# Performance work log

Hardware: AMD Instinct MI355X
Metric: run time of the kernel (lower is better)

The kernel has to match this reference:

```python
import jax, jax.numpy as jnp
import numpy as np

# static config (matches init_kwargs)
B = 16
S = 32          # patch grid side
td = 2          # tile_dim
ts = td * td    # tile size
T = (S // td) ** 2
R = 1           # register tokens
U = 1           # tile_comp_size
P = S * S
N = R + P
KC = T * U
K = R + KC
D = 768
H = 12
DH = D // H
HID = 32        # CPB hidden


def setup_inputs() -> dict:
    key = jax.random.key(0)
    ks = jax.random.split(key, 11)
    sc = 0.02
    x = jax.random.normal(ks[0], (B, N, D), jnp.float32)
    logit_w = jax.random.normal(ks[1], (U, D), jnp.float32) * sc
    q_w = jax.random.normal(ks[2], (D, D), jnp.float32) * sc
    kv_w = jax.random.normal(ks[3], (2 * D, D), jnp.float32) * sc
    out_w = jax.random.normal(ks[4], (D, D), jnp.float32) * sc
    out_b = jax.random.normal(ks[5], (D,), jnp.float32) * sc
    cpb_w1 = jax.random.normal(ks[6], (HID, 3), jnp.float32) * 0.5
    cpb_b1 = jax.random.normal(ks[7], (HID,), jnp.float32) * sc
    cpb_w2 = jax.random.normal(ks[8], (H, HID), jnp.float32) * 0.1
    cpb_b2 = jax.random.normal(ks[9], (H,), jnp.float32) * sc
    u_pos = jax.random.normal(ks[10], (1, U, 3), jnp.float32) * sc
    # query patch positions [qx, qy, 0] on the SxS grid (row-major)
    coords = np.arange(S, dtype=np.float32)
    gy, gx = np.meshgrid(coords, coords, indexing='ij')
    P_pos = np.stack([gx.ravel(), gy.ravel(), np.zeros(P, np.float32)], axis=-1)[:, None, :]
    # per-tile centers [cx, cy, 0], tile index t = row_tile*(S//td)+col_tile
    tc = np.arange(S // td, dtype=np.float32) * td + (td - 1) / 2.0
    ty, tx = np.meshgrid(tc, tc, indexing='ij')
    tile_centers = np.stack([tx.ravel(), ty.ravel(), np.zeros(T, np.float32)], axis=-1)[:, None, :]
    return {
        'x': x, 'logit_w': logit_w, 'q_w': q_w, 'kv_w': kv_w,
        'out_w': out_w, 'out_b': out_b,
        'cpb_w1': cpb_w1, 'cpb_b1': cpb_b1, 'cpb_w2': cpb_w2, 'cpb_b2': cpb_b2,
        'u_pos': u_pos,
        'P_pos': jnp.asarray(P_pos), 'tile_centers': jnp.asarray(tile_centers),
    }


def _cpb_bias(P_pos, tile_centers, u_pos, cpb_w1, cpb_b1, cpb_w2, cpb_b2, dtype):
    # anchors: tile center + tied per-U offset -> [KC, 3]
    k_pos = (tile_centers + u_pos).reshape(KC, 3)
    delta = P_pos - k_pos[None, :, :].reshape(1, KC, 3)  # [P, KC, 3]
    dxy, s_feat = delta[..., :2], delta[..., 2:]
    phi_xy = jnp.sign(dxy) * jnp.log1p(jnp.abs(dxy))
    feats = jnp.concatenate([phi_xy, -s_feat], axis=-1)  # [P, KC, 3]
    h = jax.nn.gelu(feats @ cpb_w1.T + cpb_b1, approximate=False)
    out_ctx = h @ cpb_w2.T + cpb_b2  # [P, KC, H]
    bias = jnp.zeros((N, K, H), dtype).at[R:, R:, :].set(out_ctx.astype(dtype))
    return bias.transpose(2, 0, 1)  # [H, N, K]


def reference(x, logit_w, q_w, kv_w, out_w, out_b,
              cpb_w1, cpb_b1, cpb_w2, cpb_b2, u_pos, P_pos, tile_centers):
    Bx = x.shape[0]
    # --- tiled softmax-weighted compression ---
    patch = x[:, R:, :].reshape(Bx, S // td, td, S // td, td, D)
    tiled = patch.transpose(0, 1, 3, 2, 4, 5).reshape(Bx, T, ts, D)  # [B,T,ts,D]
    scores = jnp.einsum('btsd,ud->btsu', tiled, logit_w)             # [B,T,ts,U]
    w = jax.nn.softmax(scores.astype(jnp.float32).transpose(0, 1, 3, 2), axis=-1)
    w = w.astype(scores.dtype)                                       # [B,T,U,ts]
    ctx_learn = jnp.einsum('btus,btsd->btud', w, tiled).reshape(Bx, T * U, D)
    ctx = jnp.concatenate([x[:, :R, :], ctx_learn], axis=1)          # [B,K,D]
    # --- projections ---
    q = jnp.einsum('bnd,ed->bne', x, q_w).reshape(Bx, N, H, DH).transpose(0, 2, 1, 3)
    kv = jnp.einsum('bkd,ed->bke', ctx, kv_w).reshape(Bx, K, 2, H, DH)
    k = kv[:, :, 0].transpose(0, 2, 1, 3)  # [B,H,K,DH]
    v = kv[:, :, 1].transpose(0, 2, 1, 3)
    # --- CPB additive bias + SDPA ---
    bias = _cpb_bias(P_pos, tile_centers, u_pos, cpb_w1, cpb_b1, cpb_w2, cpb_b2, x.dtype)
    scale = DH ** -0.5
    logits = jnp.einsum('bhnd,bhkd->bhnk', q, k) * scale + bias[None]
    attn = jax.nn.softmax(logits, axis=-1)
    o = jnp.einsum('bhnk,bhkd->bhnd', attn, v).transpose(0, 2, 1, 3).reshape(Bx, N, D)
    return o @ out_w.T + out_b
```

## Files before the change

kernel.cpp:

```cpp
#include <hip/hip_runtime.h>
#include <math.h>

namespace {
constexpr int BB   = 16;
constexpr int SS   = 32;
constexpr int TT   = 256;
constexpr int PP   = 1024;
constexpr int NTOK = 1025;
constexpr int KCC  = 256;
constexpr int KTOK = 257;
constexpr int DD   = 768;
constexpr int HH   = 12;
constexpr int DHH  = 64;
constexpr int BNP  = 1040;
}

typedef _Float16 f16x8 __attribute__((ext_vector_type(8)));
typedef _Float16 f16x2 __attribute__((ext_vector_type(2)));
typedef float f32x4 __attribute__((ext_vector_type(4)));

#define GLOAD_LDS16(gsrc, ldst)                                               \
  __builtin_amdgcn_global_load_lds(                                           \
      (const __attribute__((address_space(1))) unsigned int*)(gsrc),          \
      (__attribute__((address_space(3))) unsigned int*)(ldst), 16, 0, 0)

__global__ __launch_bounds__(256) void cvt_weights_kernel(
    const float* __restrict__ q_w, const float* __restrict__ kv_w,
    const float* __restrict__ out_w,
    _Float16* __restrict__ qwh, _Float16* __restrict__ kvwh,
    _Float16* __restrict__ owh) {
  constexpr int NQ = DD * DD;
  constexpr int NK = 2 * DD * DD;
  const int i = (blockIdx.x * 256 + threadIdx.x) * 8;
  const float* src;
  _Float16* dst;
  int off;
  float scale = 1.0f;
  if (i < NQ) { src = q_w; dst = qwh; off = i; scale = 0.125f; }
  else if (i < NQ + NK) { src = kv_w; dst = kvwh; off = i - NQ; }
  else if (i < NQ + NK + NQ) { src = out_w; dst = owh; off = i - NQ - NK; }
  else return;
  const float4 a = *(const float4*)(src + off);
  const float4 b = *(const float4*)(src + off + 4);
  f16x8 o;
  o[0] = (_Float16)(a.x * scale); o[1] = (_Float16)(a.y * scale);
  o[2] = (_Float16)(a.z * scale); o[3] = (_Float16)(a.w * scale);
  o[4] = (_Float16)(b.x * scale); o[5] = (_Float16)(b.y * scale);
  o[6] = (_Float16)(b.z * scale); o[7] = (_Float16)(b.w * scale);
  *(f16x8*)(dst + off) = o;
}

__global__ __launch_bounds__(256) void ctx_kernel(
    const float* __restrict__ x, const float* __restrict__ logit_w,
    _Float16* __restrict__ ctxh, _Float16* __restrict__ xh) {
  const int blk = blockIdx.x;
  const int b = blk >> 8;
  const int t = blk & 255;
  const int tid = threadIdx.x;
  const int lane = tid & 63;
  const int w = tid >> 6;
  const float* xb = x + (size_t)b * NTOK * DD;
  _Float16* xhb = xh + (size_t)b * NTOK * DD;

  int prow[4];
#pragma unroll
  for (int s = 0; s < 4; ++s)
    prow[s] = 1 + ((t >> 4) * 2 + (s >> 1)) * SS + ((t & 15) * 2 + (s & 1));

  float sv[3][4];
  float part[4] = {0.f, 0.f, 0.f, 0.f};
#pragma unroll
  for (int it = 0; it < 3; ++it) {
    const int d = tid + 256 * it;
    const float lw = logit_w[d];
#pragma unroll
    for (int s = 0; s < 4; ++s) {
      const float xv = xb[(size_t)prow[s] * DD + d];
      sv[it][s] = xv;
      part[s] += xv * lw;
      xhb[(size_t)prow[s] * DD + d] = (_Float16)xv;
    }
  }

#pragma unroll
  for (int dd = 1; dd < 64; dd <<= 1)
#pragma unroll
    for (int s = 0; s < 4; ++s) part[s] += __shfl_xor(part[s], dd, 64);
  __shared__ float wred[4][4];
  if (lane == 0)
#pragma unroll
    for (int s = 0; s < 4; ++s) wred[w][s] = part[s];
  __syncthreads();
  float score[4];
#pragma unroll
  for (int s = 0; s < 4; ++s)
    score[s] = wred[0][s] + wred[1][s] + wred[2][s] + wred[3][s];

  const float mx = fmaxf(fmaxf(score[0], score[1]), fmaxf(score[2], score[3]));
  float e[4], sum = 0.f;
#pragma unroll
  for (int s = 0; s < 4; ++s) { e[s] = expf(score[s] - mx); sum += e[s]; }
  const float inv = 1.f / sum;
#pragma unroll
  for (int s = 0; s < 4; ++s) e[s] *= inv;

  _Float16* crow = ctxh + ((size_t)b * KTOK + 1 + t) * DD;
#pragma unroll
  for (int it = 0; it < 3; ++it) {
    const int d = tid + 256 * it;
    float acc = 0.f;
#pragma unroll
    for (int s = 0; s < 4; ++s) acc += e[s] * sv[it][s];
    crow[d] = (_Float16)acc;
  }
  if (t == 0) {
    _Float16* dst = ctxh + (size_t)b * KTOK * DD;
#pragma unroll
    for (int it = 0; it < 3; ++it) {
      const int d = tid + 256 * it;
      const float xv = xb[d];
      dst[d] = (_Float16)xv;
      xhb[d] = (_Float16)xv;
    }
  }
}

template <int OUTF16>
__global__ __launch_bounds__(256) void gemm_f16_kernel(
    const _Float16* __restrict__ A, const _Float16* __restrict__ W,
    const float* __restrict__ bias, void* __restrict__ Cout,
    int M, int Nout, int gx) {
  constexpr int BK = 64;
  __shared__ _Float16 As[128 * BK];
  __shared__ _Float16 Ws[128 * BK];

  const int tid = threadIdx.x;
  const int lane = tid & 63;
  const int w = tid >> 6;
  const int fr = lane & 15;
  const int g = lane >> 4;
  const int awm = (w >> 1) * 64;
  const int awn = (w & 1) * 64;

  const int nwg = gridDim.x;
  const int q8 = nwg >> 3, r8 = nwg & 7;
  const int xcd = blockIdx.x & 7;
  const int base = (xcd < r8) ? xcd * (q8 + 1) : r8 * (q8 + 1) + (xcd - r8) * q8;
  const int wg = base + (blockIdx.x >> 3);
  const int row0 = (wg / gx) * 128;
  const int col0 = (wg % gx) * 128;

  const int srow = lane >> 3;
  const int schunk = (lane & 7) ^ (srow & 7);

  f32x4 acc[4][4];
#pragma unroll
  for (int i = 0; i < 4; ++i)
#pragma unroll
    for (int j = 0; j < 4; ++j) acc[i][j] = (f32x4){0.f, 0.f, 0.f, 0.f};

  for (int k0 = 0; k0 < 768; k0 += BK) {
    __syncthreads();
#pragma unroll
    for (int c = 0; c < 4; ++c) {
      const int rl = w * 32 + c * 8 + srow;
      int ga = row0 + rl;
      ga = ga < M ? ga : M - 1;
      GLOAD_LDS16(A + (size_t)ga * 768 + k0 + schunk * 8, &As[(w * 32 + c * 8) * BK]);
      GLOAD_LDS16(W + (size_t)(col0 + rl) * 768 + k0 + schunk * 8,
                  &Ws[(w * 32 + c * 8) * BK]);
    }
    __syncthreads();

#pragma unroll
    for (int ks = 0; ks < 2; ++ks) {
      f16x8 af[4], bf[4];
#pragma unroll
      for (int i = 0; i < 4; ++i) {
        const int row = awm + i * 16 + fr;
        af[i] = *(const f16x8*)&As[row * BK + (((ks * 4 + g) ^ (fr & 7)) * 8)];
      }
#pragma unroll
      for (int j = 0; j < 4; ++j) {
        const int row = awn + j * 16 + fr;
        bf[j] = *(const f16x8*)&Ws[row * BK + (((ks * 4 + g) ^ (fr & 7)) * 8)];
      }
#pragma unroll
      for (int i = 0; i < 4; ++i)
#pragma unroll
        for (int j = 0; j < 4; ++j)
          acc[i][j] = __builtin_amdgcn_mfma_f32_16x16x32_f16(af[i], bf[j], acc[i][j], 0, 0, 0);
    }
  }

#pragma unroll
  for (int i = 0; i < 4; ++i) {
    const int rbase = row0 + awm + i * 16 + g * 4;
#pragma unroll
    for (int reg = 0; reg < 4; ++reg) {
      const int gr = rbase + reg;
      if (gr >= M) continue;
      if constexpr (OUTF16) {
        _Float16* crow = (_Float16*)Cout + (size_t)gr * Nout + col0;
#pragma unroll
        for (int j = 0; j < 4; ++j)
          crow[awn + j * 16 + fr] = (_Float16)acc[i][j][reg];
      } else {
        float* crow = (float*)Cout + (size_t)gr * Nout + col0;
#pragma unroll
        for (int j = 0; j < 4; ++j) {
          const int gc = awn + j * 16 + fr;
          crow[gc] = acc[i][j][reg] + bias[col0 + gc];
        }
      }
    }
  }
}

__global__ __launch_bounds__(256) void cpb_kernel(
    const float* __restrict__ P_pos, const float* __restrict__ tile_centers,
    const float* __restrict__ u_pos,
    const float* __restrict__ w1, const float* __restrict__ b1,
    const float* __restrict__ w2, const float* __restrict__ b2,
    float* __restrict__ biasK) {
  const int idx = blockIdx.x * 256 + threadIdx.x;
  const int c = idx >> 10;
  const int p = idx & 1023;

  const float px = P_pos[p * 3 + 0], py = P_pos[p * 3 + 1], pz = P_pos[p * 3 + 2];
  const float kx = tile_centers[c * 3 + 0] + u_pos[0];
  const float ky = tile_centers[c * 3 + 1] + u_pos[1];
  const float kz = tile_centers[c * 3 + 2] + u_pos[2];
  const float dx = px - kx, dy = py - ky, dz = pz - kz;
  const float fx = copysignf(log1pf(fabsf(dx)), dx);
  const float fy = copysignf(log1pf(fabsf(dy)), dy);
  const float fz = -dz;

  float outh[HH];
#pragma unroll
  for (int h = 0; h < HH; ++h) outh[h] = b2[h];
  for (int j = 0; j < 32; ++j) {
    float hj = fx * w1[j * 3 + 0] + fy * w1[j * 3 + 1] + fz * w1[j * 3 + 2] + b1[j];
    hj = 0.5f * hj * (1.f + erff(hj * 0.70710678118654752f));
#pragma unroll
    for (int h = 0; h < HH; ++h) outh[h] += hj * w2[h * 32 + j];
  }
#pragma unroll
  for (int h = 0; h < HH; ++h) {
    float* row = biasK + ((size_t)h * KCC + c) * BNP;
    row[1 + p] = outh[h];
    if (p == 0) row[0] = 0.f;
    if (p < BNP - 1 - PP) row[1 + PP + p] = 0.f;
  }
}

__global__ __launch_bounds__(256) void attn_mfma_kernel(
    const _Float16* __restrict__ qf, const _Float16* __restrict__ kvf,
    const float* __restrict__ biasK, _Float16* __restrict__ of) {
  __shared__ _Float16 Kh[64 * 64];
  __shared__ _Float16 Vt[64 * 64];
  __shared__ _Float16 Pl[4][16 * 64];

  const int tid = threadIdx.x;
  const int lane = tid & 63;
  const int w = tid >> 6;
  const int fr = lane & 15;
  const int g = lane >> 4;

  const int bid = blockIdx.x;
  const int xcd = bid & 7;
  const int slot = bid >> 3;
  const int j9 = slot / 9;
  const int m = slot - 9 * j9;
  const int grp = xcd + 8 * j9;
  const int b = grp / HH;
  const int h = grp % HH;
  const int q0 = m * 128;

  f16x8 qa[2][2];
#pragma unroll
  for (int i = 0; i < 2; ++i) {
    const int qrow = min(q0 + w * 32 + i * 16 + fr, NTOK - 1);
    const _Float16* src = qf + ((size_t)b * NTOK + qrow) * DD + h * DHH;
#pragma unroll
    for (int ks = 0; ks < 2; ++ks)
      qa[i][ks] = *(const f16x8*)(src + ks * 32 + g * 8);
  }

  float mr_[2][4], lr_[2][4];
#pragma unroll
  for (int i = 0; i < 2; ++i)
#pragma unroll
    for (int r = 0; r < 4; ++r) { mr_[i][r] = -3.0e38f; lr_[i][r] = 0.f; }
  f32x4 outacc[2][4];
#pragma unroll
  for (int i = 0; i < 2; ++i)
#pragma unroll
    for (int j = 0; j < 4; ++j) outacc[i][j] = (f32x4){0.f, 0.f, 0.f, 0.f};

  const int ksr = tid >> 2;
  const int kc0 = (tid & 3) * 2;
  const int vkp = tid & 31;
  const int vdh = (tid >> 5) * 8;
  const int s7 = ksr & 7;

  for (int kt = 0; kt < 4; ++kt) {
    const int k0 = kt * 64;
    __syncthreads();
    {
      const int key = k0 + ksr;
      const _Float16* srcK = kvf + ((size_t)b * KTOK + key) * (2 * DD) + h * DHH;
      *(f16x8*)&Kh[ksr * 64 + ((kc0 ^ s7) * 8)] = *(const f16x8*)(srcK + kc0 * 8);
      *(f16x8*)&Kh[ksr * 64 + (((kc0 + 1) ^ s7) * 8)] = *(const f16x8*)(srcK + kc0 * 8 + 8);
      const int kv0 = k0 + 2 * vkp;
      const f16x8 va = *(const f16x8*)(kvf + ((size_t)b * KTOK + kv0) * (2 * DD) + DD + h * DHH + vdh);
      const f16x8 vbv = *(const f16x8*)(kvf + ((size_t)b * KTOK + kv0 + 1) * (2 * DD) + DD + h * DHH + vdh);
#pragma unroll
      for (int e = 0; e < 8; ++e) {
        const int d = vdh + e;
        f16x2 pr; pr[0] = va[e]; pr[1] = vbv[e];
        *(f16x2*)&Vt[d * 64 + (((vkp >> 2) ^ (d & 7)) * 8) + 2 * (vkp & 3)] = pr;
      }
    }
    __syncthreads();

#pragma unroll
    for (int i = 0; i < 2; ++i) {
      f32x4 sf[4];
      __builtin_amdgcn_s_setprio(1);
#pragma unroll
      for (int f = 0; f < 4; ++f) {
        sf[f] = (f32x4){0.f, 0.f, 0.f, 0.f};
#pragma unroll
        for (int ks = 0; ks < 2; ++ks) {
          const f16x8 kf = *(const f16x8*)&Kh[(f * 16 + fr) * 64 + (((ks * 4 + g) ^ (fr & 7)) * 8)];
          sf[f] = __builtin_amdgcn_mfma_f32_16x16x32_f16(qa[i][ks], kf, sf[f], 0, 0, 0);
        }
      }
      __builtin_amdgcn_s_setprio(0);

      const int nb = min(q0 + w * 32 + i * 16 + g * 4, PP);
      float pm[4][4];
#pragma unroll
      for (int f = 0; f < 4; ++f) {
        const int key = k0 + f * 16 + fr;
        const int cl = min(max(key - 1, 0), KCC - 1);
        const f32x4 b4 = *(const f32x4*)&biasK[((size_t)h * KCC + cl) * BNP + nb];
        const float bm = (key >= 1) ? 1.f : 0.f;
#pragma unroll
        for (int r = 0; r < 4; ++r) pm[f][r] = sf[f][r] + bm * b4[r];
      }

#pragma unroll
      for (int r = 0; r < 4; ++r) {
        float rm = fmaxf(fmaxf(pm[0][r], pm[1][r]), fmaxf(pm[2][r], pm[3][r]));
#pragma unroll
        for (int d = 1; d < 16; d <<= 1) rm = fmaxf(rm, __shfl_xor(rm, d, 64));
        const float mn = fmaxf(mr_[i][r], rm);
        const float corr = __expf(mr_[i][r] - mn);
        mr_[i][r] = mn;
        float rs = 0.f;
#pragma unroll
        for (int f = 0; f < 4; ++f) {
          const float pv = __expf(pm[f][r] - mn);
          pm[f][r] = pv;
          rs += pv;
        }
#pragma unroll
        for (int d = 1; d < 16; d <<= 1) rs += __shfl_xor(rs, d, 64);
        lr_[i][r] = lr_[i][r] * corr + rs;
#pragma unroll
        for (int j = 0; j < 4; ++j) outacc[i][j][r] *= corr;
      }

#pragma unroll
      for (int f = 0; f < 4; ++f)
#pragma unroll
        for (int r = 0; r < 4; ++r) {
          const int prw = g * 4 + r;
          Pl[w][prw * 64 + (((2 * f + (fr >> 3)) ^ (prw & 7)) * 8) + (fr & 7)] =
              (_Float16)pm[f][r];
        }

      __builtin_amdgcn_s_setprio(1);
#pragma unroll
      for (int ks = 0; ks < 2; ++ks) {
        const f16x8 pa = *(const f16x8*)&Pl[w][fr * 64 + (((ks * 4 + g) ^ (fr & 7)) * 8)];
#pragma unroll
        for (int j = 0; j < 4; ++j) {
          const f16x8 vbf = *(const f16x8*)&Vt[(j * 16 + fr) * 64 + (((ks * 4 + g) ^ (fr & 7)) * 8)];
          outacc[i][j] = __builtin_amdgcn_mfma_f32_16x16x32_f16(pa, vbf, outacc[i][j], 0, 0, 0);
        }
      }
      __builtin_amdgcn_s_setprio(0);
    }
  }

  __syncthreads();
  {
    if (ksr < 16) {
      const int key = min(256 + ksr, KTOK - 1);
      const _Float16* srcK = kvf + ((size_t)b * KTOK + key) * (2 * DD) + h * DHH;
      *(f16x8*)&Kh[ksr * 64 + ((kc0 ^ s7) * 8)] = *(const f16x8*)(srcK + kc0 * 8);
      *(f16x8*)&Kh[ksr * 64 + (((kc0 + 1) ^ s7) * 8)] = *(const f16x8*)(srcK + kc0 * 8 + 8);
    }
    if (vkp < 16) {
      const int kv0 = min(256 + 2 * vkp, KTOK - 1);
      const int kv1 = min(256 + 2 * vkp + 1, KTOK - 1);
      const f16x8 va = *(const f16x8*)(kvf + ((size_t)b * KTOK + kv0) * (2 * DD) + DD + h * DHH + vdh);
      const f16x8 vbv = *(const f16x8*)(kvf + ((size_t)b * KTOK + kv1) * (2 * DD) + DD + h * DHH + vdh);
#pragma unroll
      for (int e = 0; e < 8; ++e) {
        const int d = vdh + e;
        f16x2 pr; pr[0] = va[e]; pr[1] = vbv[e];
        *(f16x2*)&Vt[d * 64 + (((vkp >> 2) ^ (d & 7)) * 8) + 2 * (vkp & 3)] = pr;
      }
    }
  }
  __syncthreads();

#pragma unroll
  for (int i = 0; i < 2; ++i) {
    f32x4 sf0 = (f32x4){0.f, 0.f, 0.f, 0.f};
#pragma unroll
    for (int ks = 0; ks < 2; ++ks) {
      const f16x8 kf = *(const f16x8*)&Kh[fr * 64 + (((ks * 4 + g) ^ (fr & 7)) * 8)];
      sf0 = __builtin_amdgcn_mfma_f32_16x16x32_f16(qa[i][ks], kf, sf0, 0, 0, 0);
    }
    const int nb = min(q0 + w * 32 + i * 16 + g * 4, PP);
    const f32x4 b4 = *(const f32x4*)&biasK[((size_t)h * KCC + (KCC - 1)) * BNP + nb];
    float pm0[4];
#pragma unroll
    for (int r = 0; r < 4; ++r)
      pm0[r] = (fr == 0) ? (sf0[r] + b4[r]) : -3.0e38f;

#pragma unroll
    for (int r = 0; r < 4; ++r) {
      float rm = pm0[r];
#pragma unroll
      for (int d = 1; d < 16; d <<= 1) rm = fmaxf(rm, __shfl_xor(rm, d, 64));
      const float mn = fmaxf(mr_[i][r], rm);
      const float corr = __expf(mr_[i][r] - mn);
      mr_[i][r] = mn;
      float pv = __expf(pm0[r] - mn);
      pm0[r] = pv;
      float rs = pv;
#pragma unroll
      for (int d = 1; d < 16; d <<= 1) rs += __shfl_xor(rs, d, 64);
      lr_[i][r] = lr_[i][r] * corr + rs;
#pragma unroll
      for (int j = 0; j < 4; ++j) outacc[i][j][r] *= corr;
    }

#pragma unroll
    for (int r = 0; r < 4; ++r) {
      const int prw = g * 4 + r;
      Pl[w][prw * 64 + (((fr >> 3) ^ (prw & 7)) * 8) + (fr & 7)] = (_Float16)pm0[r];
      Pl[w][prw * 64 + (((2 + (fr >> 3)) ^ (prw & 7)) * 8) + (fr & 7)] = (_Float16)0.f;
    }

    const f16x8 pa = *(const f16x8*)&Pl[w][fr * 64 + ((g ^ (fr & 7)) * 8)];
#pragma unroll
    for (int j = 0; j < 4; ++j) {
      const f16x8 vbf = *(const f16x8*)&Vt[(j * 16 + fr) * 64 + ((g ^ (fr & 7)) * 8)];
      outacc[i][j] = __builtin_amdgcn_mfma_f32_16x16x32_f16(pa, vbf, outacc[i][j], 0, 0, 0);
    }
  }

#pragma unroll
  for (int i = 0; i < 2; ++i)
#pragma unroll
    for (int r = 0; r < 4; ++r) {
      const int n = q0 + w * 32 + i * 16 + g * 4 + r;
      if (n >= NTOK) continue;
      const float inv = 1.f / lr_[i][r];
      _Float16* orow = of + ((size_t)b * NTOK + n) * DD + h * DHH + fr;
#pragma unroll
      for (int j = 0; j < 4; ++j) orow[j * 16] = (_Float16)(outacc[i][j][r] * inv);
    }
}

extern "C" void kernel_launch(void* const* d_in, const int* in_sizes, int n_in,
                              void* d_out, int out_size, void* d_ws, size_t ws_size,
                              hipStream_t stream) {
  const float* x            = (const float*)d_in[0];
  const float* logit_w      = (const float*)d_in[1];
  const float* q_w          = (const float*)d_in[2];
  const float* kv_w         = (const float*)d_in[3];
  const float* out_w        = (const float*)d_in[4];
  const float* out_b        = (const float*)d_in[5];
  const float* cpb_w1       = (const float*)d_in[6];
  const float* cpb_b1       = (const float*)d_in[7];
  const float* cpb_w2       = (const float*)d_in[8];
  const float* cpb_b2       = (const float*)d_in[9];
  const float* u_pos        = (const float*)d_in[10];
  const float* P_pos        = (const float*)d_in[11];
  const float* tile_centers = (const float*)d_in[12];
  float* out = (float*)d_out;

  const int Mq  = BB * NTOK;
  const int Mkv = BB * KTOK;

  char* p = (char*)d_ws;
  auto alloc = [&](size_t bytes) {
    char* r = p;
    p += (bytes + 255) & ~(size_t)255;
    return r;
  };
  _Float16* xh    = (_Float16*)alloc((size_t)Mq * DD * 2);
  _Float16* ctxh  = (_Float16*)alloc((size_t)Mkv * DD * 2);
  _Float16* qwh   = (_Float16*)alloc((size_t)DD * DD * 2);
  _Float16* kvwh  = (_Float16*)alloc((size_t)2 * DD * DD * 2);
  _Float16* owh   = (_Float16*)alloc((size_t)DD * DD * 2);
  _Float16* qbuf  = (_Float16*)alloc((size_t)Mq * DD * 2);
  _Float16* kvbuf = (_Float16*)alloc((size_t)Mkv * 2 * DD * 2);
  float*    biasK = (float*)alloc((size_t)HH * KCC * BNP * 4);
  _Float16* obuf  = (_Float16*)alloc((size_t)Mq * DD * 2);

  const int n_wt = 4 * DD * DD;

  cvt_weights_kernel<<<(n_wt / 8 + 255) / 256, 256, 0, stream>>>(
      q_w, kv_w, out_w, qwh, kvwh, owh);

  ctx_kernel<<<BB * TT, 256, 0, stream>>>(x, logit_w, ctxh, xh);

  const int gq = 6 * 129;
  const int gk = 12 * 33;
  gemm_f16_kernel<1><<<gq, 256, 0, stream>>>(xh, qwh, nullptr, qbuf, Mq, DD, 6);
  gemm_f16_kernel<1><<<gk, 256, 0, stream>>>(ctxh, kvwh, nullptr, kvbuf, Mkv, 2 * DD, 12);

  cpb_kernel<<<(PP * KCC) / 256, 256, 0, stream>>>(
      P_pos, tile_centers, u_pos, cpb_w1, cpb_b1, cpb_w2, cpb_b2, biasK);

  attn_mfma_kernel<<<8 * 216, 256, 0, stream>>>(
      qbuf, kvbuf, biasK, obuf);

  gemm_f16_kernel<0><<<gq, 256, 0, stream>>>(obuf, owh, out_b, out, Mq, DD, 6);
}
```

Baseline: 215.2 us.

## Load full per-head K/V once into LDS and loop waves over query chunks

The attention kernel now launches one 512-thread block per (batch, head). It stages all 257 keys and the transposed values in LDS once, with one barrier, and each of the 8 waves then loops over 16-row query chunks. This removes the repeated K/V loads and the per-tile barriers that every 128-query block paid. In exchange the grid shrinks to 192 blocks on a GPU with many CUs, and LDS use grows to about 88KB per block, which lowers occupancy and leaves the last chunk round unevenly balanced.

```diff
diff --git a/kernel.cpp b/kernel.cpp
--- a/kernel.cpp
+++ b/kernel.cpp
@@ -254,12 +254,14 @@
   }
 }
 
-__global__ __launch_bounds__(256) void attn_mfma_kernel(
+__global__ __launch_bounds__(512) void attn_mfma_kernel(
     const _Float16* __restrict__ qf, const _Float16* __restrict__ kvf,
     const float* __restrict__ biasK, _Float16* __restrict__ of) {
-  __shared__ _Float16 Kh[64 * 64];
-  __shared__ _Float16 Vt[64 * 64];
-  __shared__ _Float16 Pl[4][16 * 64];
+  __shared__ _Float16 Kh[4][64 * 64];
+  __shared__ _Float16 Kt[16 * 64];
+  __shared__ _Float16 Vt[4][64 * 64];
+  __shared__ _Float16 Vtt[64 * 64];
+  __shared__ _Float16 Pl[8][16 * 64];
 
   const int tid = threadIdx.x;
   const int lane = tid & 63;
@@ -267,65 +269,79 @@
   const int fr = lane & 15;
   const int g = lane >> 4;
 
-  const int bid = blockIdx.x;
-  const int xcd = bid & 7;
-  const int slot = bid >> 3;
-  const int j9 = slot / 9;
-  const int m = slot - 9 * j9;
-  const int grp = xcd + 8 * j9;
-  const int b = grp / HH;
-  const int h = grp % HH;
-  const int q0 = m * 128;
-
-  f16x8 qa[2][2];
-#pragma unroll
-  for (int i = 0; i < 2; ++i) {
-    const int qrow = min(q0 + w * 32 + i * 16 + fr, NTOK - 1);
-    const _Float16* src = qf + ((size_t)b * NTOK + qrow) * DD + h * DHH;
-#pragma unroll
-    for (int ks = 0; ks < 2; ++ks)
-      qa[i][ks] = *(const f16x8*)(src + ks * 32 + g * 8);
-  }
-
-  float mr_[2][4], lr_[2][4];
-#pragma unroll
-  for (int i = 0; i < 2; ++i)
-#pragma unroll
-    for (int r = 0; r < 4; ++r) { mr_[i][r] = -3.0e38f; lr_[i][r] = 0.f; }
-  f32x4 outacc[2][4];
-#pragma unroll
-  for (int i = 0; i < 2; ++i)
-#pragma unroll
-    for (int j = 0; j < 4; ++j) outacc[i][j] = (f32x4){0.f, 0.f, 0.f, 0.f};
-
-  const int ksr = tid >> 2;
-  const int kc0 = (tid & 3) * 2;
-  const int vkp = tid & 31;
-  const int vdh = (tid >> 5) * 8;
-  const int s7 = ksr & 7;
-
-  for (int kt = 0; kt < 4; ++kt) {
-    const int k0 = kt * 64;
-    __syncthreads();
-    {
-      const int key = k0 + ksr;
+  const int b = blockIdx.x / HH;
+  const int h = blockIdx.x % HH;
+
+  if (tid < 256) {
+    const int ksr = tid >> 2;
+    const int kc0 = (tid & 3) * 2;
+    const int s7 = ksr & 7;
+#pragma unroll
+    for (int kt = 0; kt < 4; ++kt) {
+      const int key = kt * 64 + ksr;
       const _Float16* srcK = kvf + ((size_t)b * KTOK + key) * (2 * DD) + h * DHH;
-      *(f16x8*)&Kh[ksr * 64 + ((kc0 ^ s7) * 8)] = *(const f16x8*)(srcK + kc0 * 8);
-      *(f16x8*)&Kh[ksr * 64 + (((kc0 + 1) ^ s7) * 8)] = *(const f16x8*)(srcK + kc0 * 8 + 8);
-      const int kv0 = k0 + 2 * vkp;
+      *(f16x8*)&Kh[kt][ksr * 64 + ((kc0 ^ s7) * 8)] = *(const f16x8*)(srcK + kc0 * 8);
+      *(f16x8*)&Kh[kt][ksr * 64 + (((kc0 + 1) ^ s7) * 8)] = *(const f16x8*)(srcK + kc0 * 8 + 8);
+    }
+    if (ksr < 16) {
+      const int key = min(256 + ksr, KTOK - 1);
+      const _Float16* srcK = kvf + ((size_t)b * KTOK + key) * (2 * DD) + h * DHH;
+      *(f16x8*)&Kt[ksr * 64 + ((kc0 ^ s7) * 8)] = *(const f16x8*)(srcK + kc0 * 8);
+      *(f16x8*)&Kt[ksr * 64 + (((kc0 + 1) ^ s7) * 8)] = *(const f16x8*)(srcK + kc0 * 8 + 8);
+    }
+  } else {
+    const int t2 = tid - 256;
+    const int vkp = t2 & 31;
+    const int vdh = (t2 >> 5) * 8;
+#pragma unroll
+    for (int kt = 0; kt < 4; ++kt) {
+      const int kv0 = kt * 64 + 2 * vkp;
       const f16x8 va = *(const f16x8*)(kvf + ((size_t)b * KTOK + kv0) * (2 * DD) + DD + h * DHH + vdh);
       const f16x8 vbv = *(const f16x8*)(kvf + ((size_t)b * KTOK + kv0 + 1) * (2 * DD) + DD + h * DHH + vdh);
 #pragma unroll
       for (int e = 0; e < 8; ++e) {
         const int d = vdh + e;
         f16x2 pr; pr[0] = va[e]; pr[1] = vbv[e];
-        *(f16x2*)&Vt[d * 64 + (((vkp >> 2) ^ (d & 7)) * 8) + 2 * (vkp & 3)] = pr;
-      }
-    }
-    __syncthreads();
-
-#pragma unroll
-    for (int i = 0; i < 2; ++i) {
+        *(f16x2*)&Vt[kt][d * 64 + (((vkp >> 2) ^ (d & 7)) * 8) + 2 * (vkp & 3)] = pr;
+      }
+    }
+    if (vkp < 16) {
+      const int kv0 = min(256 + 2 * vkp, KTOK - 1);
+      const int kv1 = min(256 + 2 * vkp + 1, KTOK - 1);
+      const f16x8 va = *(const f16x8*)(kvf + ((size_t)b * KTOK + kv0) * (2 * DD) + DD + h * DHH + vdh);
+      const f16x8 vbv = *(const f16x8*)(kvf + ((size_t)b * KTOK + kv1) * (2 * DD) + DD + h * DHH + vdh);
+#pragma unroll
+      for (int e = 0; e < 8; ++e) {
+        const int d = vdh + e;
+        f16x2 pr; pr[0] = va[e]; pr[1] = vbv[e];
+        *(f16x2*)&Vtt[d * 64 + (((vkp >> 2) ^ (d & 7)) * 8) + 2 * (vkp & 3)] = pr;
+      }
+    }
+  }
+  __syncthreads();
+
+  for (int c = w; c < 65; c += 8) {
+    const int qc = c * 16;
+
+    const int qrow = min(qc + fr, NTOK - 1);
+    const _Float16* qsrc = qf + ((size_t)b * NTOK + qrow) * DD + h * DHH;
+    f16x8 qa[2];
+#pragma unroll
+    for (int ks = 0; ks < 2; ++ks)
+      qa[ks] = *(const f16x8*)(qsrc + ks * 32 + g * 8);
+
+    float mr_[4], lr_[4];
+#pragma unroll
+    for (int r = 0; r < 4; ++r) { mr_[r] = -3.0e38f; lr_[r] = 0.f; }
+    f32x4 outacc[4];
+#pragma unroll
+    for (int j = 0; j < 4; ++j) outacc[j] = (f32x4){0.f, 0.f, 0.f, 0.f};
+
+    const int nb = min(qc + g * 4, PP);
+
+#pragma unroll
+    for (int kt = 0; kt < 4; ++kt) {
+      const int k0 = kt * 64;
       f32x4 sf[4];
       __builtin_amdgcn_s_setprio(1);
 #pragma unroll
@@ -333,13 +349,12 @@
         sf[f] = (f32x4){0.f, 0.f, 0.f, 0.f};
 #pragma unroll
         for (int ks = 0; ks < 2; ++ks) {
-          const f16x8 kf = *(const f16x8*)&Kh[(f * 16 + fr) * 64 + (((ks * 4 + g) ^ (fr & 7)) * 8)];
-          sf[f] = __builtin_amdgcn_mfma_f32_16x16x32_f16(qa[i][ks], kf, sf[f], 0, 0, 0);
+          const f16x8 kf = *(const f16x8*)&Kh[kt][(f * 16 + fr) * 64 + (((ks * 4 + g) ^ (fr & 7)) * 8)];
+          sf[f] = __builtin_amdgcn_mfma_f32_16x16x32_f16(qa[ks], kf, sf[f], 0, 0, 0);
         }
       }
       __builtin_amdgcn_s_setprio(0);
 
-      const int nb = min(q0 + w * 32 + i * 16 + g * 4, PP);
       float pm[4][4];
 #pragma unroll
       for (int f = 0; f < 4; ++f) {
@@ -356,9 +371,9 @@
         float rm = fmaxf(fmaxf(pm[0][r], pm[1][r]), fmaxf(pm[2][r], pm[3][r]));
 #pragma unroll
         for (int d = 1; d < 16; d <<= 1) rm = fmaxf(rm, __shfl_xor(rm, d, 64));
-        const float mn = fmaxf(mr_[i][r], rm);
-        const float corr = __expf(mr_[i][r] - mn);
-        mr_[i][r] = mn;
+        const float mn = fmaxf(mr_[r], rm);
+        const float corr = __expf(mr_[r] - mn);
+        mr_[r] = mn;
         float rs = 0.f;
 #pragma unroll
         for (int f = 0; f < 4; ++f) {
@@ -368,9 +383,9 @@
         }
 #pragma unroll
         for (int d = 1; d < 16; d <<= 1) rs += __shfl_xor(rs, d, 64);
-        lr_[i][r] = lr_[i][r] * corr + rs;
-#pragma unroll
-        for (int j = 0; j < 4; ++j) outacc[i][j][r] *= corr;
+        lr_[r] = lr_[r] * corr + rs;
+#pragma unroll
+        for (int j = 0; j < 4; ++j) outacc[j][r] *= corr;
       }
 
 #pragma unroll
@@ -388,96 +403,69 @@
         const f16x8 pa = *(const f16x8*)&Pl[w][fr * 64 + (((ks * 4 + g) ^ (fr & 7)) * 8)];
 #pragma unroll
         for (int j = 0; j < 4; ++j) {
-          const f16x8 vbf = *(const f16x8*)&Vt[(j * 16 + fr) * 64 + (((ks * 4 + g) ^ (fr & 7)) * 8)];
-          outacc[i][j] = __builtin_amdgcn_mfma_f32_16x16x32_f16(pa, vbf, outacc[i][j], 0, 0, 0);
+          const f16x8 vbf = *(const f16x8*)&Vt[kt][(j * 16 + fr) * 64 + (((ks * 4 + g) ^ (fr & 7)) * 8)];
+          outacc[j] = __builtin_amdgcn_mfma_f32_16x16x32_f16(pa, vbf, outacc[j], 0, 0, 0);
         }
       }
       __builtin_amdgcn_s_setprio(0);
     }
-  }
-
-  __syncthreads();
-  {
-    if (ksr < 16) {
-      const int key = min(256 + ksr, KTOK - 1);
-      const _Float16* srcK = kvf + ((size_t)b * KTOK + key) * (2 * DD) + h * DHH;
-      *(f16x8*)&Kh[ksr * 64 + ((kc0 ^ s7) * 8)] = *(const f16x8*)(srcK + kc0 * 8);
-      *(f16x8*)&Kh[ksr * 64 + (((kc0 + 1) ^ s7) * 8)] = *(const f16x8*)(srcK + kc0 * 8 + 8);
-    }
-    if (vkp < 16) {
-      const int kv0 = min(256 + 2 * vkp, KTOK - 1);
-      const int kv1 = min(256 + 2 * vkp + 1, KTOK - 1);
-      const f16x8 va = *(const f16x8*)(kvf + ((size_t)b * KTOK + kv0) * (2 * DD) + DD + h * DHH + vdh);
-      const f16x8 vbv = *(const f16x8*)(kvf + ((size_t)b * KTOK + kv1) * (2 * DD) + DD + h * DHH + vdh);
-#pragma unroll
-      for (int e = 0; e < 8; ++e) {
-        const int d = vdh + e;
-        f16x2 pr; pr[0] = va[e]; pr[1] = vbv[e];
-        *(f16x2*)&Vt[d * 64 + (((vkp >> 2) ^ (d & 7)) * 8) + 2 * (vkp & 3)] = pr;
-      }
-    }
-  }
-  __syncthreads();
-
-#pragma unroll
-  for (int i = 0; i < 2; ++i) {
-    f32x4 sf0 = (f32x4){0.f, 0.f, 0.f, 0.f};
-#pragma unroll
-    for (int ks = 0; ks < 2; ++ks) {
-      const f16x8 kf = *(const f16x8*)&Kh[fr * 64 + (((ks * 4 + g) ^ (fr & 7)) * 8)];
-      sf0 = __builtin_amdgcn_mfma_f32_16x16x32_f16(qa[i][ks], kf, sf0, 0, 0, 0);
-    }
-    const int nb = min(q0 + w * 32 + i * 16 + g * 4, PP);
-    const f32x4 b4 = *(const f32x4*)&biasK[((size_t)h * KCC + (KCC - 1)) * BNP + nb];
-    float pm0[4];
-#pragma unroll
-    for (int r = 0; r < 4; ++r)
-      pm0[r] = (fr == 0) ? (sf0[r] + b4[r]) : -3.0e38f;
+
+    {
+      f32x4 sf0 = (f32x4){0.f, 0.f, 0.f, 0.f};
+#pragma unroll
+      for (int ks = 0; ks < 2; ++ks) {
+        const f16x8 kf = *(const f16x8*)&Kt[fr * 64 + (((ks * 4 + g) ^ (fr & 7)) * 8)];
+        sf0 = __builtin_amdgcn_mfma_f32_16x16x32_f16(qa[ks], kf, sf0, 0, 0, 0);
+      }
+      const f32x4 b4 = *(const f32x4*)&biasK[((size_t)h * KCC + (KCC - 1)) * BNP + nb];
+      float pm0[4];
+#pragma unroll
+      for (int r = 0; r < 4; ++r)
+        pm0[r] = (fr == 0) ? (sf0[r] + b4[r]) : -3.0e38f;
+
+#pragma unroll
+      for (int r = 0; r < 4; ++r) {
+        float rm = pm0[r];
+#pragma unroll
+        for (int d = 1; d < 16; d <<= 1) rm = fmaxf(rm, __shfl_xor(rm, d, 64));
+        const float mn = fmaxf(mr_[r], rm);
+        const float corr = __expf(mr_[r] - mn);
+        mr_[r] = mn;
+        float pv = __expf(pm0[r] - mn);
+        pm0[r] = pv;
+        float rs = pv;
+#pragma unroll
+        for (int d = 1; d < 16; d <<= 1) rs += __shfl_xor(rs, d, 64);
+        lr_[r] = lr_[r] * corr + rs;
+#pragma unroll
+        for (int j = 0; j < 4; ++j) outacc[j][r] *= corr;
+      }
+
+#pragma unroll
+      for (int r = 0; r < 4; ++r) {
+        const int prw = g * 4 + r;
+        Pl[w][prw * 64 + (((fr >> 3) ^ (prw & 7)) * 8) + (fr & 7)] = (_Float16)pm0[r];
+        Pl[w][prw * 64 + (((2 + (fr >> 3)) ^ (prw & 7)) * 8) + (fr & 7)] = (_Float16)0.f;
+      }
+
+      const f16x8 pa = *(const f16x8*)&Pl[w][fr * 64 + ((g ^ (fr & 7)) * 8)];
+#pragma unroll
+      for (int j = 0; j < 4; ++j) {
+        const f16x8 vbf = *(const f16x8*)&Vtt[(j * 16 + fr) * 64 + ((g ^ (fr & 7)) * 8)];
+        outacc[j] = __builtin_amdgcn_mfma_f32_16x16x32_f16(pa, vbf, outacc[j], 0, 0, 0);
+      }
+    }
 
 #pragma unroll
     for (int r = 0; r < 4; ++r) {
-      float rm = pm0[r];
-#pragma unroll
-      for (int d = 1; d < 16; d <<= 1) rm = fmaxf(rm, __shfl_xor(rm, d, 64));
-      const float mn = fmaxf(mr_[i][r], rm);
-      const float corr = __expf(mr_[i][r] - mn);
-      mr_[i][r] = mn;
-      float pv = __expf(pm0[r] - mn);
-      pm0[r] = pv;
-      float rs = pv;
-#pragma unroll
-      for (int d = 1; d < 16; d <<= 1) rs += __shfl_xor(rs, d, 64);
-      lr_[i][r] = lr_[i][r] * corr + rs;
-#pragma unroll
-      for (int j = 0; j < 4; ++j) outacc[i][j][r] *= corr;
-    }
-
-#pragma unroll
-    for (int r = 0; r < 4; ++r) {
-      const int prw = g * 4 + r;
-      Pl[w][prw * 64 + (((fr >> 3) ^ (prw & 7)) * 8) + (fr & 7)] = (_Float16)pm0[r];
-      Pl[w][prw * 64 + (((2 + (fr >> 3)) ^ (prw & 7)) * 8) + (fr & 7)] = (_Float16)0.f;
-    }
-
-    const f16x8 pa = *(const f16x8*)&Pl[w][fr * 64 + ((g ^ (fr & 7)) * 8)];
-#pragma unroll
-    for (int j = 0; j < 4; ++j) {
-      const f16x8 vbf = *(const f16x8*)&Vt[(j * 16 + fr) * 64 + ((g ^ (fr & 7)) * 8)];
-      outacc[i][j] = __builtin_amdgcn_mfma_f32_16x16x32_f16(pa, vbf, outacc[i][j], 0, 0, 0);
-    }
-  }
-
-#pragma unroll
-  for (int i = 0; i < 2; ++i)
-#pragma unroll
-    for (int r = 0; r < 4; ++r) {
-      const int n = q0 + w * 32 + i * 16 + g * 4 + r;
+      const int n = qc + g * 4 + r;
       if (n >= NTOK) continue;
-      const float inv = 1.f / lr_[i][r];
+      const float inv = 1.f / lr_[r];
       _Float16* orow = of + ((size_t)b * NTOK + n) * DD + h * DHH + fr;
 #pragma unroll
-      for (int j = 0; j < 4; ++j) orow[j * 16] = (_Float16)(outacc[i][j][r] * inv);
-    }
+      for (int j = 0; j < 4; ++j) orow[j * 16] = (_Float16)(outacc[j][r] * inv);
+    }
+  }
 }
 
 extern "C" void kernel_launch(void* const* d_in, const int* in_sizes, int n_in,
@@ -532,8 +520,7 @@
   cpb_kernel<<<(PP * KCC) / 256, 256, 0, stream>>>(
       P_pos, tile_centers, u_pos, cpb_w1, cpb_b1, cpb_w2, cpb_b2, biasK);
 
-  attn_mfma_kernel<<<8 * 216, 256, 0, stream>>>(
-      qbuf, kvbuf, biasK, obuf);
+  attn_mfma_kernel<<<BB * HH, 512, 0, stream>>>(qbuf, kvbuf, biasK, obuf);
 
   gemm_f16_kernel<0><<<gq, 256, 0, stream>>>(obuf, owh, out_b, out, Mq, DD, 6);
 }
```

Result: faster. 198.9 us (-7.6%).
